# Kernel tuning notes

Hardware: AMD Instinct MI355X
Metric: run time of the kernel (lower is better)

The kernel has to match this reference:

```python
import jax, jax.numpy as jnp
import numpy as np

N = 50000        # nodes
E = 200000       # interior edges
EB = 40000       # boundary edges
WID = 32         # hidden width
KER = 6          # edge feature dim
DEPTH = 4


def setup_inputs() -> dict:
    key = jax.random.key(0)
    ks = jax.random.split(key, 24)
    f32 = jnp.float32

    def nrm(k, sh, s):
        return jax.random.normal(k, sh, dtype=f32) * s

    inp = {
        "x": nrm(ks[0], (N, 1), 1.0),
        "edge_index": jax.random.randint(ks[1], (2, E), 0, N),
        "edge_attr": jax.random.uniform(ks[2], (E, KER), dtype=f32),
        "edge_index_boundary": jax.random.randint(ks[3], (2, EB), 0, N),
        "edge_attr_boundary": jax.random.uniform(ks[4], (EB, KER), dtype=f32),
        # fc1: in_width=1 -> width
        "fc1_w": nrm(ks[5], (1, WID), 0.3), "fc1_b": jnp.zeros((WID,), f32),
        # kernel MLP 1: [6 -> 8 -> 32 -> 32*32], ReLU between layers, none at end
        "k1_w1": nrm(ks[6], (KER, WID // 4), 0.3), "k1_b1": jnp.zeros((WID // 4,), f32),
        "k1_w2": nrm(ks[7], (WID // 4, WID), 0.2), "k1_b2": jnp.zeros((WID,), f32),
        "k1_w3": nrm(ks[8], (WID, WID * WID), 0.05), "k1_b3": jnp.zeros((WID * WID,), f32),
        # kernel MLP 2 (boundary)
        "k2_w1": nrm(ks[9], (KER, WID // 4), 0.3), "k2_b1": jnp.zeros((WID // 4,), f32),
        "k2_w2": nrm(ks[10], (WID // 4, WID), 0.2), "k2_b2": jnp.zeros((WID,), f32),
        "k2_w3": nrm(ks[11], (WID, WID * WID), 0.05), "k2_b3": jnp.zeros((WID * WID,), f32),
        # NNConv root weights + biases
        "root1": nrm(ks[12], (WID, WID), 0.15), "bias1": jnp.zeros((WID,), f32),
        "root2": nrm(ks[13], (WID, WID), 0.15), "bias2": jnp.zeros((WID,), f32),
        # fc2: width -> 1
        "fc2_w": nrm(ks[14], (WID, 1), 0.2), "fc2_b": jnp.zeros((1,), f32),
    }
    return inp


def _kernel_mlp(ea, w1, b1, w2, b2, w3, b3):
    # DenseNet: ReLU between layers, no final nonlinearity -> per-edge [W, W] matrices
    h = jax.nn.relu(ea @ w1 + b1)
    h = jax.nn.relu(h @ w2 + b2)
    return (h @ w3 + b3).reshape(-1, WID, WID)


def _nnconv(x, src, dst, We, root, bias):
    # message: gather x_j then per-edge matmul  [E, W] x [E, W, W] -> [E, W]
    msg = jnp.einsum('ei,eio->eo', x[src], We)
    agg = jax.ops.segment_sum(msg, dst, num_segments=N)
    cnt = jax.ops.segment_sum(jnp.ones((src.shape[0], 1), msg.dtype), dst, num_segments=N)
    mean = agg / jnp.maximum(cnt, 1.0)  # isolated nodes -> 0
    return mean + x @ root + bias


def reference(x, edge_index, edge_attr, edge_index_boundary, edge_attr_boundary,
              fc1_w, fc1_b,
              k1_w1, k1_b1, k1_w2, k1_b2, k1_w3, k1_b3,
              k2_w1, k2_b1, k2_w2, k2_b2, k2_w3, k2_b3,
              root1, bias1, root2, bias2,
              fc2_w, fc2_b):
    src, dst = edge_index[0], edge_index[1]
    srcb, dstb = edge_index_boundary[0], edge_index_boundary[1]
    # edge-conditioned weight matrices are x-independent: hoist out of depth loop
    W1 = _kernel_mlp(edge_attr, k1_w1, k1_b1, k1_w2, k1_b2, k1_w3, k1_b3)
    W2 = _kernel_mlp(edge_attr_boundary, k2_w1, k2_b1, k2_w2, k2_b2, k2_w3, k2_b3)

    h = x @ fc1_w + fc1_b  # [N, W]
    for _ in range(DEPTH):
        h = jax.nn.relu(_nnconv(h, src, dst, W1, root1, bias1)
                        + _nnconv(h, srcb, dstb, W2, root2, bias2))
    return h @ fc2_w + fc2_b  # [N, 1]
```

## Files before the change

### kernel.cpp

```cpp
#include <hip/hip_runtime.h>
#include <hip/hip_bf16.h>

#define WID 32
#define KER 6
#define DEPTH 4
#define WEXT_ELEMS (33 * 2 * 64 * 8)

typedef __attribute__((ext_vector_type(8))) short bf16x8;
typedef __attribute__((ext_vector_type(4))) float f32x4;

static __device__ __forceinline__ float bf2f(unsigned short u) {
  union { unsigned int u; float f; } v; v.u = ((unsigned int)u) << 16; return v.f;
}
static __device__ __forceinline__ unsigned short f2bf(float f) {
  union { float f; unsigned int u; } v; v.f = f;
  unsigned int r = v.u + 0x7fffu + ((v.u >> 16) & 1u);
  return (unsigned short)(r >> 16);
}

__global__ void k_h0(const float* __restrict__ x, const float* __restrict__ w,
                     const float* __restrict__ b, float* __restrict__ h,
                     unsigned short* __restrict__ hbf, int n_nodes) {
  int gid = blockIdx.x * blockDim.x + threadIdx.x;
  if (gid >= n_nodes * WID) return;
  int n = gid >> 5, o = gid & 31;
  float v = x[n] * w[o] + b[o];
  h[gid] = v;
  hbf[gid] = f2bf(v);
}

__global__ void k_cnt(const int* __restrict__ ei, int E,
                      const int* __restrict__ eib, int EB,
                      unsigned int* __restrict__ cnt1, unsigned int* __restrict__ cnt2,
                      unsigned int* __restrict__ rank1, unsigned int* __restrict__ rank2) {
  int idx = blockIdx.x * blockDim.x + threadIdx.x;
  if (idx < E) {
    rank1[idx] = atomicAdd(&cnt1[ei[E + idx]], 1u);
  } else if (idx < E + EB) {
    int e = idx - E;
    rank2[e] = atomicAdd(&cnt2[eib[EB + e]], 1u);
  }
}

__global__ void k_scan1(const unsigned int* __restrict__ cnt, unsigned int* __restrict__ partials,
                        int n2) {
  __shared__ unsigned int s[256];
  int t = threadIdx.x;
  int i = blockIdx.x * 256 + t;
  unsigned int v = (i < n2) ? cnt[i] : 0u;
  s[t] = v;
  __syncthreads();
  for (int d = 128; d > 0; d >>= 1) {
    if (t < d) s[t] += s[t + d];
    __syncthreads();
  }
  if (t == 0) partials[blockIdx.x] = s[0];
}

__global__ void k_scan2(unsigned int* __restrict__ partials, int nb) {
  __shared__ unsigned int s[1024];
  int t = threadIdx.x;
  unsigned int v = (t < nb) ? partials[t] : 0u;
  s[t] = v;
  __syncthreads();
  for (int d = 1; d < 1024; d <<= 1) {
    unsigned int u = (t >= d) ? s[t - d] : 0u;
    __syncthreads();
    s[t] += u;
    __syncthreads();
  }
  if (t < nb) partials[t] = s[t] - v;
}

__global__ void k_scan3(const unsigned int* __restrict__ cnt, const unsigned int* __restrict__ partials,
                        unsigned int* __restrict__ start1, unsigned int* __restrict__ start2,
                        int n, int Etot) {
  __shared__ unsigned int s[256];
  int t = threadIdx.x;
  int i = blockIdx.x * 256 + t;
  int n2 = 2 * n;
  unsigned int v = (i < n2) ? cnt[i] : 0u;
  s[t] = v;
  __syncthreads();
  for (int d = 1; d < 256; d <<= 1) {
    unsigned int u = (t >= d) ? s[t - d] : 0u;
    __syncthreads();
    s[t] += u;
    __syncthreads();
  }
  unsigned int ex = s[t] - v + partials[blockIdx.x];
  if (i < n) start1[i] = ex;
  else if (i < n2) start2[i - n] = ex - (unsigned int)Etot;
}

__global__ void k_edgemlp(const float* __restrict__ ea,
                          const int* __restrict__ eidx, int ecnt,
                          const unsigned int* __restrict__ rank,
                          const unsigned int* __restrict__ start,
                          const float* __restrict__ w1, const float* __restrict__ b1,
                          const float* __restrict__ w2, const float* __restrict__ b2,
                          unsigned short* __restrict__ h3s, int* __restrict__ ssrc) {
  __shared__ float sw1[KER * 8], sb1[8], sw2[8 * WID], sb2[WID];
  int tid = threadIdx.x;
  if (tid < KER * 8) sw1[tid] = w1[tid];
  if (tid < 8) sb1[tid] = b1[tid];
  if (tid < 8 * WID) sw2[tid] = w2[tid];
  if (tid < WID) sb2[tid] = b2[tid];
  __syncthreads();
  int e = blockIdx.x * blockDim.x + tid;
  if (e >= ecnt) return;
  float a[KER];
  #pragma unroll
  for (int i = 0; i < KER; i++) a[i] = ea[e * KER + i];
  float h8[8];
  #pragma unroll
  for (int o = 0; o < 8; o++) {
    float s = sb1[o];
    #pragma unroll
    for (int i = 0; i < KER; i++) s += a[i] * sw1[i * 8 + o];
    h8[o] = fmaxf(s, 0.f);
  }
  int d = eidx[ecnt + e];
  unsigned int p = start[d] + rank[e];
  ssrc[p] = eidx[e];
  size_t base = (size_t)p * WID;
  #pragma unroll
  for (int o = 0; o < WID; o++) {
    float s = sb2[o];
    #pragma unroll
    for (int i = 0; i < 8; i++) s += h8[i] * sw2[i * WID + o];
    h3s[base + o] = f2bf(fmaxf(s, 0.f));
  }
}

__global__ void k_pack2(const float* __restrict__ w3a, const float* __restrict__ b3a,
                        unsigned short* __restrict__ oa,
                        const float* __restrict__ w3b, const float* __restrict__ b3b,
                        unsigned short* __restrict__ ob) {
  int idx = blockIdx.x * blockDim.x + threadIdx.x;
  if (idx >= 2 * WEXT_ELEMS) return;
  int which = idx >= WEXT_ELEMS;
  int id2 = which ? idx - WEXT_ELEMS : idx;
  const float* w3 = which ? w3b : w3a;
  const float* b3 = which ? b3b : b3a;
  unsigned short* outp = which ? ob : oa;
  int j = id2 & 7, l = (id2 >> 3) & 63, tt = (id2 >> 9) & 1, s = id2 >> 10;
  int p = ((l >> 4) << 3) + j;
  int o = tt * 16 + (l & 15);
  float v = (s < 32) ? w3[s * 1024 + p * 32 + o] : b3[p * 32 + o];
  outp[id2] = f2bf(v);
}

__launch_bounds__(512)
__global__ void k_msg2(const unsigned short* __restrict__ hbf,
                       const unsigned short* __restrict__ h3s1, const int* __restrict__ ssrc1,
                       int ecnt1, const unsigned short* __restrict__ w1,
                       unsigned short* __restrict__ msg1,
                       const unsigned short* __restrict__ h3s2, const int* __restrict__ ssrc2,
                       int ecnt2, const unsigned short* __restrict__ w2,
                       unsigned short* __restrict__ msg2, int B1) {
  const unsigned short* h3s; const int* ssrc; const unsigned short* wext;
  unsigned short* msgbuf; int ecnt, blk0, nblk;
  if ((int)blockIdx.x < B1) {
    h3s = h3s1; ssrc = ssrc1; wext = w1; msgbuf = msg1; ecnt = ecnt1;
    blk0 = blockIdx.x; nblk = B1;
  } else {
    h3s = h3s2; ssrc = ssrc2; wext = w2; msgbuf = msg2; ecnt = ecnt2;
    blk0 = blockIdx.x - B1; nblk = gridDim.x - B1;
  }
  __shared__ __align__(16) unsigned short wlds[WEXT_ELEMS];
  {
    const uint4* s4 = (const uint4*)wext;
    uint4* d4 = (uint4*)wlds;
    for (int i = threadIdx.x; i < WEXT_ELEMS / 8; i += blockDim.x) d4[i] = s4[i];
  }
  __syncthreads();
  const int lane = threadIdx.x & 63;
  const int wv = threadIdx.x >> 6;
  const int g = lane >> 4, eo = lane & 15;
  const int ntile = (ecnt + 15) >> 4;
  const int wpb = blockDim.x >> 6;
  const int nwv = nblk * wpb;
  for (int tile = blk0 * wpb + wv; tile < ntile; tile += nwv) {
    const int e = min((tile << 4) + eo, ecnt - 1);
    const int srcn = ssrc[e];
    const uint4* h3p = (const uint4*)(h3s + (size_t)e * WID);
    uint4 q0 = h3p[0], q1 = h3p[1], q2 = h3p[2], q3 = h3p[3];
    unsigned int h3w[16];
    h3w[0]=q0.x; h3w[1]=q0.y; h3w[2]=q0.z; h3w[3]=q0.w;
    h3w[4]=q1.x; h3w[5]=q1.y; h3w[6]=q1.z; h3w[7]=q1.w;
    h3w[8]=q2.x; h3w[9]=q2.y; h3w[10]=q2.z; h3w[11]=q2.w;
    h3w[12]=q3.x; h3w[13]=q3.y; h3w[14]=q3.z; h3w[15]=q3.w;
    uint4 hq = *(const uint4*)(hbf + (size_t)srcn * WID + g * 8);
    bf16x8 hsv = __builtin_bit_cast(bf16x8, hq);
    float hsf[8];
    #pragma unroll
    for (int j = 0; j < 8; j++) hsf[j] = bf2f((unsigned short)hsv[j]);
    f32x4 acc0 = {0.f, 0.f, 0.f, 0.f};
    f32x4 acc1 = {0.f, 0.f, 0.f, 0.f};
    #pragma unroll
    for (int s = 0; s < 32; s++) {
      unsigned int wrd = h3w[s >> 1];
      unsigned int fb = (s & 1) ? (wrd & 0xffff0000u) : (wrd << 16);
      float h3f = __builtin_bit_cast(float, fb);
      float p0 = h3f * hsf[0], p1 = h3f * hsf[1], p2 = h3f * hsf[2], p3 = h3f * hsf[3];
      float p4 = h3f * hsf[4], p5 = h3f * hsf[5], p6 = h3f * hsf[6], p7 = h3f * hsf[7];
      uint4 aw;
      asm("v_cvt_pk_bf16_f32 %0, %1, %2" : "=v"(aw.x) : "v"(p0), "v"(p1));
      asm("v_cvt_pk_bf16_f32 %0, %1, %2" : "=v"(aw.y) : "v"(p2), "v"(p3));
      asm("v_cvt_pk_bf16_f32 %0, %1, %2" : "=v"(aw.z) : "v"(p4), "v"(p5));
      asm("v_cvt_pk_bf16_f32 %0, %1, %2" : "=v"(aw.w) : "v"(p6), "v"(p7));
      bf16x8 af = __builtin_bit_cast(bf16x8, aw);
      bf16x8 b0 = *(const bf16x8*)&wlds[((s * 2 + 0) * 64 + lane) * 8];
      bf16x8 b1 = *(const bf16x8*)&wlds[((s * 2 + 1) * 64 + lane) * 8];
      acc0 = __builtin_amdgcn_mfma_f32_16x16x32_bf16(af, b0, acc0, 0, 0, 0);
      acc1 = __builtin_amdgcn_mfma_f32_16x16x32_bf16(af, b1, acc1, 0, 0, 0);
    }
    {
      bf16x8 b0 = *(const bf16x8*)&wlds[((32 * 2 + 0) * 64 + lane) * 8];
      bf16x8 b1 = *(const bf16x8*)&wlds[((32 * 2 + 1) * 64 + lane) * 8];
      acc0 = __builtin_amdgcn_mfma_f32_16x16x32_bf16(hsv, b0, acc0, 0, 0, 0);
      acc1 = __builtin_amdgcn_mfma_f32_16x16x32_bf16(hsv, b1, acc1, 0, 0, 0);
    }
    #pragma unroll
    for (int r = 0; r < 4; r++) {
      int oe = (tile << 4) + g * 4 + r;
      if (oe < ecnt) {
        msgbuf[(size_t)oe * WID + eo]      = f2bf(acc0[r]);
        msgbuf[(size_t)oe * WID + 16 + eo] = f2bf(acc1[r]);
      }
    }
  }
}

__global__ void k_update(const unsigned short* __restrict__ msg1,
                         const unsigned short* __restrict__ msg2,
                         const unsigned int* __restrict__ start1, const unsigned int* __restrict__ cnt1,
                         const unsigned int* __restrict__ start2, const unsigned int* __restrict__ cnt2,
                         const float* __restrict__ root1, const float* __restrict__ root2,
                         const float* __restrict__ bias1, const float* __restrict__ bias2,
                         float* __restrict__ h, unsigned short* __restrict__ hbf,
                         int last, const float* __restrict__ fc2w, const float* __restrict__ fc2b,
                         float* __restrict__ out, int n_nodes) {
  __shared__ float rs[WID * WID];
  __shared__ float bs[WID];
  __shared__ float hrow[8][WID];
  int tid = threadIdx.x;
  for (int i = tid; i < WID * WID; i += blockDim.x) rs[i] = root1[i] + root2[i];
  if (tid < WID) bs[tid] = bias1[tid] + bias2[tid];
  int o = tid & 31, nl = tid >> 5;
  int n = blockIdx.x * 8 + nl;
  bool ok = (n < n_nodes);
  hrow[nl][o] = ok ? h[(size_t)n * WID + o] : 0.f;
  __syncthreads();
  if (!ok) return;
  unsigned int b1 = start1[n], c1 = cnt1[n];
  unsigned int b2 = start2[n], c2 = cnt2[n];
  float s1 = 0.f, s2 = 0.f;
  for (unsigned int k = 0; k < c1; k++) s1 += bf2f(msg1[(size_t)(b1 + k) * WID + o]);
  for (unsigned int k = 0; k < c2; k++) s2 += bf2f(msg2[(size_t)(b2 + k) * WID + o]);
  float v = s1 / (float)(c1 ? c1 : 1u) + s2 / (float)(c2 ? c2 : 1u) + bs[o];
  #pragma unroll
  for (int i = 0; i < WID; i++) v += hrow[nl][i] * rs[i * WID + o];
  v = fmaxf(v, 0.f);
  h[(size_t)n * WID + o] = v;
  hbf[(size_t)n * WID + o] = f2bf(v);
  if (last) {
    float pv = v * fc2w[o];
    #pragma unroll
    for (int m = 16; m >= 1; m >>= 1) pv += __shfl_xor(pv, m, 32);
    if (o == 0) out[n] = pv + fc2b[0];
  }
}

extern "C" void kernel_launch(void* const* d_in, const int* in_sizes, int n_in,
                              void* d_out, int out_size, void* d_ws, size_t ws_size,
                              hipStream_t stream) {
  const float* x    = (const float*)d_in[0];
  const int*   ei   = (const int*)d_in[1];
  const float* ea   = (const float*)d_in[2];
  const int*   eib  = (const int*)d_in[3];
  const float* eab  = (const float*)d_in[4];
  const float* fc1w = (const float*)d_in[5];
  const float* fc1b = (const float*)d_in[6];
  const float* k1w1 = (const float*)d_in[7];
  const float* k1b1 = (const float*)d_in[8];
  const float* k1w2 = (const float*)d_in[9];
  const float* k1b2 = (const float*)d_in[10];
  const float* k1w3 = (const float*)d_in[11];
  const float* k1b3 = (const float*)d_in[12];
  const float* k2w1 = (const float*)d_in[13];
  const float* k2b1 = (const float*)d_in[14];
  const float* k2w2 = (const float*)d_in[15];
  const float* k2b2 = (const float*)d_in[16];
  const float* k2w3 = (const float*)d_in[17];
  const float* k2b3 = (const float*)d_in[18];
  const float* root1 = (const float*)d_in[19];
  const float* bias1 = (const float*)d_in[20];
  const float* root2 = (const float*)d_in[21];
  const float* bias2 = (const float*)d_in[22];
  const float* fc2w = (const float*)d_in[23];
  const float* fc2b = (const float*)d_in[24];
  float* out = (float*)d_out;

  const int n_nodes = in_sizes[0];
  const int E  = in_sizes[1] / 2;
  const int EB = in_sizes[3] / 2;

  char* ws = (char*)d_ws;
  size_t off = 0;
  auto alloc = [&](size_t bytes) -> void* {
    void* p = ws + off;
    off = (off + bytes + 255) & ~(size_t)255;
    return p;
  };
  unsigned short* h3s1 = (unsigned short*)alloc((size_t)E * WID * 2);
  unsigned short* h3s2 = (unsigned short*)alloc((size_t)EB * WID * 2);
  unsigned short* w1b  = (unsigned short*)alloc((size_t)WEXT_ELEMS * 2);
  unsigned short* w2b  = (unsigned short*)alloc((size_t)WEXT_ELEMS * 2);
  float* h             = (float*)alloc((size_t)n_nodes * WID * 4);
  unsigned short* hbf  = (unsigned short*)alloc((size_t)n_nodes * WID * 2);
  unsigned short* msg1 = (unsigned short*)alloc((size_t)E * WID * 2);
  unsigned short* msg2 = (unsigned short*)alloc((size_t)EB * WID * 2);
  unsigned int* cnt12  = (unsigned int*)alloc((size_t)2 * n_nodes * 4);
  unsigned int* cnt1 = cnt12;
  unsigned int* cnt2 = cnt12 + n_nodes;
  unsigned int* start1 = (unsigned int*)alloc((size_t)n_nodes * 4);
  unsigned int* start2 = (unsigned int*)alloc((size_t)n_nodes * 4);
  unsigned int* rank1  = (unsigned int*)alloc((size_t)E * 4);
  unsigned int* rank2  = (unsigned int*)alloc((size_t)EB * 4);
  int* ssrc1 = (int*)alloc((size_t)E * 4);
  int* ssrc2 = (int*)alloc((size_t)EB * 4);
  unsigned int* partials = (unsigned int*)alloc((size_t)1024 * 4);
  (void)ws_size; (void)n_in; (void)out_size;

  const int n2 = 2 * n_nodes;
  const int nb = (n2 + 255) / 256;

  hipMemsetAsync(cnt12, 0, (size_t)n2 * 4, stream);
  int tot = E + EB;
  k_cnt<<<(tot + 255) / 256, 256, 0, stream>>>(ei, E, eib, EB, cnt1, cnt2, rank1, rank2);
  k_scan1<<<nb, 256, 0, stream>>>(cnt12, partials, n2);
  k_scan2<<<1, 1024, 0, stream>>>(partials, nb);
  k_scan3<<<nb, 256, 0, stream>>>(cnt12, partials, start1, start2, n_nodes, E);
  k_h0<<<(n_nodes * WID + 255) / 256, 256, 0, stream>>>(x, fc1w, fc1b, h, hbf, n_nodes);
  k_edgemlp<<<(E + 255) / 256, 256, 0, stream>>>(ea, ei, E, rank1, start1,
                                                 k1w1, k1b1, k1w2, k1b2, h3s1, ssrc1);
  k_edgemlp<<<(EB + 255) / 256, 256, 0, stream>>>(eab, eib, EB, rank2, start2,
                                                  k2w1, k2b1, k2w2, k2b2, h3s2, ssrc2);
  k_pack2<<<(2 * WEXT_ELEMS + 255) / 256, 256, 0, stream>>>(k1w3, k1b3, w1b, k2w3, k2b3, w2b);

  const int GRID = 512;
  int B1 = (int)(((long long)GRID * E) / (E + EB));
  if (B1 < 1) B1 = 1;
  if (B1 > GRID - 1) B1 = GRID - 1;

  for (int t = 0; t < DEPTH; t++) {
    k_msg2<<<GRID, 512, 0, stream>>>(hbf, h3s1, ssrc1, E, w1b, msg1,
                                     h3s2, ssrc2, EB, w2b, msg2, B1);
    int last = (t == DEPTH - 1);
    k_update<<<(n_nodes + 7) / 8, 256, 0, stream>>>(msg1, msg2, start1, cnt1, start2, cnt2,
                                                    root1, root2, bias1, bias2, h, hbf,
                                                    last, fc2w, fc2b, out, n_nodes);
  }
}
```

Measured before the change: 339.8 us.

## Fuse whole GNN pipeline into cooperative persistent megakernel with grid syncs

Replaces the chain of setup, edge-MLP, pack, message and update kernels with a single cooperative kernel (256 blocks × 512 threads). The phases are separated by grid-wide syncs, and the old launch path is kept as a fallback if the cooperative launch fails. The message stage now processes 32-edge supertiles per wave, sharing the LDS weight fragments across two 16-edge MFMA tiles. The aim is to remove launch gaps and inter-kernel drain between the many small stages. In exchange it adds grid-barrier cost and limits the grid to 256 blocks. The fused update phase also reads h rows from global memory rather than staging them in LDS, which may make it slower than the separate update kernel.

Measured after the change: 854.1 us. 2.51x slower.

```diff
diff --git a/kernel.cpp b/kernel.cpp
--- a/kernel.cpp
+++ b/kernel.cpp
@@ -1,10 +1,15 @@
 #include <hip/hip_runtime.h>
 #include <hip/hip_bf16.h>
+#include <hip/hip_cooperative_groups.h>
+
+namespace cg = cooperative_groups;
 
 #define WID 32
 #define KER 6
 #define DEPTH 4
 #define WEXT_ELEMS (33 * 2 * 64 * 8)
+#define NB 256
+#define NT 512
 
 typedef __attribute__((ext_vector_type(8))) short bf16x8;
 typedef __attribute__((ext_vector_type(4))) float f32x4;
@@ -16,6 +21,271 @@
   union { float f; unsigned int u; } v; v.f = f;
   unsigned int r = v.u + 0x7fffu + ((v.u >> 16) & 1u);
   return (unsigned short)(r >> 16);
+}
+
+static __device__ __forceinline__ void msg_supertile(
+    const unsigned short* __restrict__ hbf, const unsigned short* __restrict__ h3s,
+    const int* __restrict__ ssrc, int ecnt, unsigned short* __restrict__ msgbuf,
+    const unsigned short* wlds, int st, int lane) {
+  const int g = lane >> 4, eo = lane & 15;
+  const int ebase = st * 32;
+  int eA = min(ebase + eo, ecnt - 1);
+  int eB = min(ebase + 16 + eo, ecnt - 1);
+  const uint4* hA = (const uint4*)(h3s + (size_t)eA * WID);
+  const uint4* hB = (const uint4*)(h3s + (size_t)eB * WID);
+  uint4 qa0 = hA[0], qa1 = hA[1], qa2 = hA[2], qa3 = hA[3];
+  uint4 qb0 = hB[0], qb1 = hB[1], qb2 = hB[2], qb3 = hB[3];
+  unsigned int hwA[16], hwB[16];
+  hwA[0]=qa0.x; hwA[1]=qa0.y; hwA[2]=qa0.z; hwA[3]=qa0.w;
+  hwA[4]=qa1.x; hwA[5]=qa1.y; hwA[6]=qa1.z; hwA[7]=qa1.w;
+  hwA[8]=qa2.x; hwA[9]=qa2.y; hwA[10]=qa2.z; hwA[11]=qa2.w;
+  hwA[12]=qa3.x; hwA[13]=qa3.y; hwA[14]=qa3.z; hwA[15]=qa3.w;
+  hwB[0]=qb0.x; hwB[1]=qb0.y; hwB[2]=qb0.z; hwB[3]=qb0.w;
+  hwB[4]=qb1.x; hwB[5]=qb1.y; hwB[6]=qb1.z; hwB[7]=qb1.w;
+  hwB[8]=qb2.x; hwB[9]=qb2.y; hwB[10]=qb2.z; hwB[11]=qb2.w;
+  hwB[12]=qb3.x; hwB[13]=qb3.y; hwB[14]=qb3.z; hwB[15]=qb3.w;
+  int srcA = ssrc[eA], srcB = ssrc[eB];
+  uint4 ha4 = *(const uint4*)(hbf + (size_t)srcA * WID + g * 8);
+  uint4 hb4 = *(const uint4*)(hbf + (size_t)srcB * WID + g * 8);
+  bf16x8 hsvA = __builtin_bit_cast(bf16x8, ha4);
+  bf16x8 hsvB = __builtin_bit_cast(bf16x8, hb4);
+  float hfA[8], hfB[8];
+  #pragma unroll
+  for (int j = 0; j < 8; j++) { hfA[j] = bf2f((unsigned short)hsvA[j]); hfB[j] = bf2f((unsigned short)hsvB[j]); }
+  f32x4 accA0 = {0.f,0.f,0.f,0.f}, accA1 = {0.f,0.f,0.f,0.f};
+  f32x4 accB0 = {0.f,0.f,0.f,0.f}, accB1 = {0.f,0.f,0.f,0.f};
+  #pragma unroll
+  for (int s = 0; s < 32; s++) {
+    unsigned int wa = hwA[s >> 1], wb = hwB[s >> 1];
+    unsigned int fa = (s & 1) ? (wa & 0xffff0000u) : (wa << 16);
+    unsigned int fbm = (s & 1) ? (wb & 0xffff0000u) : (wb << 16);
+    float h3A = __builtin_bit_cast(float, fa);
+    float h3B = __builtin_bit_cast(float, fbm);
+    float a0 = h3A*hfA[0], a1 = h3A*hfA[1], a2 = h3A*hfA[2], a3 = h3A*hfA[3];
+    float a4 = h3A*hfA[4], a5 = h3A*hfA[5], a6 = h3A*hfA[6], a7 = h3A*hfA[7];
+    float c0 = h3B*hfB[0], c1 = h3B*hfB[1], c2 = h3B*hfB[2], c3 = h3B*hfB[3];
+    float c4 = h3B*hfB[4], c5 = h3B*hfB[5], c6 = h3B*hfB[6], c7 = h3B*hfB[7];
+    uint4 awA, awB;
+    asm("v_cvt_pk_bf16_f32 %0, %1, %2" : "=v"(awA.x) : "v"(a0), "v"(a1));
+    asm("v_cvt_pk_bf16_f32 %0, %1, %2" : "=v"(awA.y) : "v"(a2), "v"(a3));
+    asm("v_cvt_pk_bf16_f32 %0, %1, %2" : "=v"(awA.z) : "v"(a4), "v"(a5));
+    asm("v_cvt_pk_bf16_f32 %0, %1, %2" : "=v"(awA.w) : "v"(a6), "v"(a7));
+    asm("v_cvt_pk_bf16_f32 %0, %1, %2" : "=v"(awB.x) : "v"(c0), "v"(c1));
+    asm("v_cvt_pk_bf16_f32 %0, %1, %2" : "=v"(awB.y) : "v"(c2), "v"(c3));
+    asm("v_cvt_pk_bf16_f32 %0, %1, %2" : "=v"(awB.z) : "v"(c4), "v"(c5));
+    asm("v_cvt_pk_bf16_f32 %0, %1, %2" : "=v"(awB.w) : "v"(c6), "v"(c7));
+    bf16x8 afA = __builtin_bit_cast(bf16x8, awA);
+    bf16x8 afB = __builtin_bit_cast(bf16x8, awB);
+    bf16x8 w0 = *(const bf16x8*)&wlds[((s * 2 + 0) * 64 + lane) * 8];
+    bf16x8 w1 = *(const bf16x8*)&wlds[((s * 2 + 1) * 64 + lane) * 8];
+    accA0 = __builtin_amdgcn_mfma_f32_16x16x32_bf16(afA, w0, accA0, 0, 0, 0);
+    accA1 = __builtin_amdgcn_mfma_f32_16x16x32_bf16(afA, w1, accA1, 0, 0, 0);
+    accB0 = __builtin_amdgcn_mfma_f32_16x16x32_bf16(afB, w0, accB0, 0, 0, 0);
+    accB1 = __builtin_amdgcn_mfma_f32_16x16x32_bf16(afB, w1, accB1, 0, 0, 0);
+  }
+  {
+    bf16x8 w0 = *(const bf16x8*)&wlds[((32 * 2 + 0) * 64 + lane) * 8];
+    bf16x8 w1 = *(const bf16x8*)&wlds[((32 * 2 + 1) * 64 + lane) * 8];
+    accA0 = __builtin_amdgcn_mfma_f32_16x16x32_bf16(hsvA, w0, accA0, 0, 0, 0);
+    accA1 = __builtin_amdgcn_mfma_f32_16x16x32_bf16(hsvA, w1, accA1, 0, 0, 0);
+    accB0 = __builtin_amdgcn_mfma_f32_16x16x32_bf16(hsvB, w0, accB0, 0, 0, 0);
+    accB1 = __builtin_amdgcn_mfma_f32_16x16x32_bf16(hsvB, w1, accB1, 0, 0, 0);
+  }
+  #pragma unroll
+  for (int r = 0; r < 4; r++) {
+    int oeA = ebase + g * 4 + r;
+    int oeB = ebase + 16 + g * 4 + r;
+    if (oeA < ecnt) {
+      msgbuf[(size_t)oeA * WID + eo]      = f2bf(accA0[r]);
+      msgbuf[(size_t)oeA * WID + 16 + eo] = f2bf(accA1[r]);
+    }
+    if (oeB < ecnt) {
+      msgbuf[(size_t)oeB * WID + eo]      = f2bf(accB0[r]);
+      msgbuf[(size_t)oeB * WID + 16 + eo] = f2bf(accB1[r]);
+    }
+  }
+}
+
+struct MegaArgs {
+  const float *x; const int *ei; const float *ea; const int *eib; const float *eab;
+  const float *fc1w, *fc1b;
+  const float *k1w1, *k1b1, *k1w2, *k1b2, *k1w3, *k1b3;
+  const float *k2w1, *k2b1, *k2w2, *k2b2, *k2w3, *k2b3;
+  const float *root1, *bias1, *root2, *bias2, *fc2w, *fc2b;
+  float* out;
+  unsigned short *h3s1, *h3s2, *w1b, *w2b, *hbf;
+  float* h;
+  unsigned short *msg1, *msg2;
+  unsigned int *cnt12, *start1, *start2, *rank1, *rank2, *partials;
+  int *ssrc1, *ssrc2;
+  int n_nodes, E, EB, B1;
+};
+
+__launch_bounds__(NT)
+__global__ void k_mega(MegaArgs a) {
+  __shared__ __align__(16) unsigned short wlds[WEXT_ELEMS];
+  __shared__ float rs[WID * WID];
+  __shared__ float bs[WID];
+  __shared__ unsigned int sscan[NT];
+  cg::grid_group grid = cg::this_grid();
+  const int tid = threadIdx.x, bid = blockIdx.x;
+  const int gtid = bid * NT + tid, gsz = NB * NT;
+  const int n_nodes = a.n_nodes, E = a.E, EB = a.EB, B1 = a.B1;
+  const int n2 = 2 * n_nodes;
+
+  for (int i = gtid; i < n2; i += gsz) a.cnt12[i] = 0u;
+  for (int i = gtid; i < n_nodes * WID; i += gsz) {
+    int n = i >> 5, o = i & 31;
+    float v = a.x[n] * a.fc1w[o] + a.fc1b[o];
+    a.h[i] = v; a.hbf[i] = f2bf(v);
+  }
+  for (int i = gtid; i < 2 * WEXT_ELEMS; i += gsz) {
+    int which = i >= WEXT_ELEMS;
+    int id2 = which ? i - WEXT_ELEMS : i;
+    const float* w3 = which ? a.k2w3 : a.k1w3;
+    const float* b3 = which ? a.k2b3 : a.k1b3;
+    unsigned short* outp = which ? a.w2b : a.w1b;
+    int j = id2 & 7, l = (id2 >> 3) & 63, tt = (id2 >> 9) & 1, s = id2 >> 10;
+    int p = ((l >> 4) << 3) + j;
+    int o = tt * 16 + (l & 15);
+    float v = (s < 32) ? w3[s * 1024 + p * 32 + o] : b3[p * 32 + o];
+    outp[id2] = f2bf(v);
+  }
+  for (int i = tid; i < WID * WID; i += NT) rs[i] = a.root1[i] + a.root2[i];
+  if (tid < WID) bs[tid] = a.bias1[tid] + a.bias2[tid];
+  grid.sync();
+
+  for (int i = gtid; i < E + EB; i += gsz) {
+    if (i < E) a.rank1[i] = atomicAdd(&a.cnt12[a.ei[E + i]], 1u);
+    else { int e = i - E; a.rank2[e] = atomicAdd(&a.cnt12[n_nodes + a.eib[EB + e]], 1u); }
+  }
+  grid.sync();
+
+  const int nbS = (n2 + NT - 1) / NT;
+  if (bid < nbS) {
+    int i = bid * NT + tid;
+    unsigned int v = (i < n2) ? a.cnt12[i] : 0u;
+    sscan[tid] = v; __syncthreads();
+    for (int d = NT / 2; d > 0; d >>= 1) { if (tid < d) sscan[tid] += sscan[tid + d]; __syncthreads(); }
+    if (tid == 0) a.partials[bid] = sscan[0];
+  }
+  grid.sync();
+  if (bid == 0) {
+    unsigned int v = (tid < nbS) ? a.partials[tid] : 0u;
+    sscan[tid] = v; __syncthreads();
+    for (int d = 1; d < NT; d <<= 1) { unsigned int u = (tid >= d) ? sscan[tid - d] : 0u; __syncthreads(); sscan[tid] += u; __syncthreads(); }
+    if (tid < nbS) a.partials[tid] = sscan[tid] - v;
+  }
+  grid.sync();
+  if (bid < nbS) {
+    int i = bid * NT + tid;
+    unsigned int v = (i < n2) ? a.cnt12[i] : 0u;
+    sscan[tid] = v; __syncthreads();
+    for (int d = 1; d < NT; d <<= 1) { unsigned int u = (tid >= d) ? sscan[tid - d] : 0u; __syncthreads(); sscan[tid] += u; __syncthreads(); }
+    unsigned int ex = sscan[tid] - v + a.partials[bid];
+    if (i < n_nodes) a.start1[i] = ex;
+    else if (i < n2) a.start2[i - n_nodes] = ex - (unsigned int)E;
+  }
+  grid.sync();
+
+  {
+    bool role1 = bid < B1;
+    const float* w1 = role1 ? a.k1w1 : a.k2w1;
+    const float* b1 = role1 ? a.k1b1 : a.k2b1;
+    const float* w2 = role1 ? a.k1w2 : a.k2w2;
+    const float* b2 = role1 ? a.k1b2 : a.k2b2;
+    float* sw = (float*)sscan;
+    if (tid < KER * 8) sw[tid] = w1[tid];
+    if (tid >= 64 && tid < 72) sw[tid] = b1[tid - 64];
+    if (tid >= 128 && tid < 384) sw[tid] = w2[tid - 128];
+    if (tid >= 384 && tid < 416) sw[tid] = b2[tid - 384];
+    __syncthreads();
+    const int ecnt = role1 ? E : EB;
+    const float* ea = role1 ? a.ea : a.eab;
+    const int* eidx = role1 ? a.ei : a.eib;
+    const unsigned int* rank = role1 ? a.rank1 : a.rank2;
+    const unsigned int* start = role1 ? a.start1 : a.start2;
+    unsigned short* h3s = role1 ? a.h3s1 : a.h3s2;
+    int* ssrc = role1 ? a.ssrc1 : a.ssrc2;
+    int blk0 = role1 ? bid : bid - B1;
+    int rblocks = role1 ? B1 : NB - B1;
+    for (int e = blk0 * NT + tid; e < ecnt; e += rblocks * NT) {
+      float aa[KER];
+      #pragma unroll
+      for (int i = 0; i < KER; i++) aa[i] = ea[e * KER + i];
+      float h8[8];
+      #pragma unroll
+      for (int o = 0; o < 8; o++) {
+        float s = sw[64 + o];
+        #pragma unroll
+        for (int i = 0; i < KER; i++) s += aa[i] * sw[i * 8 + o];
+        h8[o] = fmaxf(s, 0.f);
+      }
+      int d = eidx[ecnt + e];
+      unsigned int p = start[d] + rank[e];
+      ssrc[p] = eidx[e];
+      size_t base = (size_t)p * WID;
+      #pragma unroll
+      for (int o = 0; o < WID; o++) {
+        float s = sw[384 + o];
+        #pragma unroll
+        for (int i = 0; i < 8; i++) s += h8[i] * sw[128 + i * 32 + o];
+        h3s[base + o] = f2bf(fmaxf(s, 0.f));
+      }
+    }
+  }
+  grid.sync();
+
+  {
+    const unsigned short* wsrc = (bid < B1) ? a.w1b : a.w2b;
+    const uint4* s4 = (const uint4*)wsrc;
+    uint4* d4 = (uint4*)wlds;
+    for (int i = tid; i < WEXT_ELEMS / 8; i += NT) d4[i] = s4[i];
+  }
+  __syncthreads();
+
+  const int lane = tid & 63, wv = tid >> 6;
+  for (int t = 0; t < DEPTH; t++) {
+    {
+      bool role1 = bid < B1;
+      const unsigned short* h3s = role1 ? a.h3s1 : a.h3s2;
+      const int* ssrc = role1 ? a.ssrc1 : a.ssrc2;
+      unsigned short* msgbuf = role1 ? a.msg1 : a.msg2;
+      int ecnt = role1 ? E : EB;
+      int blk0 = role1 ? bid : bid - B1;
+      int rblocks = role1 ? B1 : NB - B1;
+      int nst = (ecnt + 31) >> 5;
+      int wpb = NT >> 6, nwv = rblocks * wpb;
+      for (int st = blk0 * wpb + wv; st < nst; st += nwv)
+        msg_supertile(a.hbf, h3s, ssrc, ecnt, msgbuf, wlds, st, lane);
+    }
+    grid.sync();
+    {
+      int last = (t == DEPTH - 1);
+      for (int idx = gtid; idx < n_nodes * WID; idx += gsz) {
+        int n = idx >> 5, o = idx & 31;
+        unsigned int b1v = a.start1[n], c1v = a.cnt12[n];
+        unsigned int b2v = a.start2[n], c2v = a.cnt12[n_nodes + n];
+        float s1 = 0.f, s2 = 0.f;
+        for (unsigned int k = 0; k < c1v; k++) s1 += bf2f(a.msg1[(size_t)(b1v + k) * WID + o]);
+        for (unsigned int k = 0; k < c2v; k++) s2 += bf2f(a.msg2[(size_t)(b2v + k) * WID + o]);
+        float v = s1 / (float)(c1v ? c1v : 1u) + s2 / (float)(c2v ? c2v : 1u) + bs[o];
+        const float* hrow = a.h + (size_t)n * WID;
+        #pragma unroll
+        for (int i = 0; i < WID; i++) v += hrow[i] * rs[i * WID + o];
+        v = fmaxf(v, 0.f);
+        a.h[idx] = v;
+        a.hbf[idx] = f2bf(v);
+        if (last) {
+          float pv = v * a.fc2w[o];
+          #pragma unroll
+          for (int m = 16; m >= 1; m >>= 1) pv += __shfl_xor(pv, m, 32);
+          if (o == 0) a.out[n] = pv + a.fc2b[0];
+        }
+      }
+    }
+    if (t < DEPTH - 1) grid.sync();
+  }
 }
 
 __global__ void k_h0(const float* __restrict__ x, const float* __restrict__ w,
@@ -158,15 +428,15 @@
                        unsigned short* __restrict__ msg1,
                        const unsigned short* __restrict__ h3s2, const int* __restrict__ ssrc2,
                        int ecnt2, const unsigned short* __restrict__ w2,
-                       unsigned short* __restrict__ msg2, int B1) {
+                       unsigned short* __restrict__ msg2, int B1f) {
   const unsigned short* h3s; const int* ssrc; const unsigned short* wext;
   unsigned short* msgbuf; int ecnt, blk0, nblk;
-  if ((int)blockIdx.x < B1) {
+  if ((int)blockIdx.x < B1f) {
     h3s = h3s1; ssrc = ssrc1; wext = w1; msgbuf = msg1; ecnt = ecnt1;
-    blk0 = blockIdx.x; nblk = B1;
+    blk0 = blockIdx.x; nblk = B1f;
   } else {
     h3s = h3s2; ssrc = ssrc2; wext = w2; msgbuf = msg2; ecnt = ecnt2;
-    blk0 = blockIdx.x - B1; nblk = gridDim.x - B1;
+    blk0 = blockIdx.x - B1f; nblk = gridDim.x - B1f;
   }
   __shared__ __align__(16) unsigned short wlds[WEXT_ELEMS];
   {
@@ -177,60 +447,11 @@
   __syncthreads();
   const int lane = threadIdx.x & 63;
   const int wv = threadIdx.x >> 6;
-  const int g = lane >> 4, eo = lane & 15;
-  const int ntile = (ecnt + 15) >> 4;
+  const int nst = (ecnt + 31) >> 5;
   const int wpb = blockDim.x >> 6;
   const int nwv = nblk * wpb;
-  for (int tile = blk0 * wpb + wv; tile < ntile; tile += nwv) {
-    const int e = min((tile << 4) + eo, ecnt - 1);
-    const int srcn = ssrc[e];
-    const uint4* h3p = (const uint4*)(h3s + (size_t)e * WID);
-    uint4 q0 = h3p[0], q1 = h3p[1], q2 = h3p[2], q3 = h3p[3];
-    unsigned int h3w[16];
-    h3w[0]=q0.x; h3w[1]=q0.y; h3w[2]=q0.z; h3w[3]=q0.w;
-    h3w[4]=q1.x; h3w[5]=q1.y; h3w[6]=q1.z; h3w[7]=q1.w;
-    h3w[8]=q2.x; h3w[9]=q2.y; h3w[10]=q2.z; h3w[11]=q2.w;
-    h3w[12]=q3.x; h3w[13]=q3.y; h3w[14]=q3.z; h3w[15]=q3.w;
-    uint4 hq = *(const uint4*)(hbf + (size_t)srcn * WID + g * 8);
-    bf16x8 hsv = __builtin_bit_cast(bf16x8, hq);
-    float hsf[8];
-    #pragma unroll
-    for (int j = 0; j < 8; j++) hsf[j] = bf2f((unsigned short)hsv[j]);
-    f32x4 acc0 = {0.f, 0.f, 0.f, 0.f};
-    f32x4 acc1 = {0.f, 0.f, 0.f, 0.f};
-    #pragma unroll
-    for (int s = 0; s < 32; s++) {
-      unsigned int wrd = h3w[s >> 1];
-      unsigned int fb = (s & 1) ? (wrd & 0xffff0000u) : (wrd << 16);
-      float h3f = __builtin_bit_cast(float, fb);
-      float p0 = h3f * hsf[0], p1 = h3f * hsf[1], p2 = h3f * hsf[2], p3 = h3f * hsf[3];
-      float p4 = h3f * hsf[4], p5 = h3f * hsf[5], p6 = h3f * hsf[6], p7 = h3f * hsf[7];
-      uint4 aw;
-      asm("v_cvt_pk_bf16_f32 %0, %1, %2" : "=v"(aw.x) : "v"(p0), "v"(p1));
-      asm("v_cvt_pk_bf16_f32 %0, %1, %2" : "=v"(aw.y) : "v"(p2), "v"(p3));
-      asm("v_cvt_pk_bf16_f32 %0, %1, %2" : "=v"(aw.z) : "v"(p4), "v"(p5));
-      asm("v_cvt_pk_bf16_f32 %0, %1, %2" : "=v"(aw.w) : "v"(p6), "v"(p7));
-      bf16x8 af = __builtin_bit_cast(bf16x8, aw);
-      bf16x8 b0 = *(const bf16x8*)&wlds[((s * 2 + 0) * 64 + lane) * 8];
-      bf16x8 b1 = *(const bf16x8*)&wlds[((s * 2 + 1) * 64 + lane) * 8];
-      acc0 = __builtin_amdgcn_mfma_f32_16x16x32_bf16(af, b0, acc0, 0, 0, 0);
-      acc1 = __builtin_amdgcn_mfma_f32_16x16x32_bf16(af, b1, acc1, 0, 0, 0);
-    }
-    {
-      bf16x8 b0 = *(const bf16x8*)&wlds[((32 * 2 + 0) * 64 + lane) * 8];
-      bf16x8 b1 = *(const bf16x8*)&wlds[((32 * 2 + 1) * 64 + lane) * 8];
-      acc0 = __builtin_amdgcn_mfma_f32_16x16x32_bf16(hsv, b0, acc0, 0, 0, 0);
-      acc1 = __builtin_amdgcn_mfma_f32_16x16x32_bf16(hsv, b1, acc1, 0, 0, 0);
-    }
-    #pragma unroll
-    for (int r = 0; r < 4; r++) {
-      int oe = (tile << 4) + g * 4 + r;
-      if (oe < ecnt) {
-        msgbuf[(size_t)oe * WID + eo]      = f2bf(acc0[r]);
-        msgbuf[(size_t)oe * WID + 16 + eo] = f2bf(acc1[r]);
-      }
-    }
-  }
+  for (int st = blk0 * wpb + wv; st < nst; st += nwv)
+    msg_supertile(hbf, h3s, ssrc, ecnt, msgbuf, wlds, st, lane);
 }
 
 __global__ void k_update(const unsigned short* __restrict__ msg1,
@@ -334,9 +555,32 @@
   unsigned int* partials = (unsigned int*)alloc((size_t)1024 * 4);
   (void)ws_size; (void)n_in; (void)out_size;
 
+  int B1c = (int)(((long long)NB * E) / (E + EB));
+  if (B1c < 1) B1c = 1;
+  if (B1c > NB - 1) B1c = NB - 1;
+
+  MegaArgs ma;
+  ma.x = x; ma.ei = ei; ma.ea = ea; ma.eib = eib; ma.eab = eab;
+  ma.fc1w = fc1w; ma.fc1b = fc1b;
+  ma.k1w1 = k1w1; ma.k1b1 = k1b1; ma.k1w2 = k1w2; ma.k1b2 = k1b2; ma.k1w3 = k1w3; ma.k1b3 = k1b3;
+  ma.k2w1 = k2w1; ma.k2b1 = k2b1; ma.k2w2 = k2w2; ma.k2b2 = k2b2; ma.k2w3 = k2w3; ma.k2b3 = k2b3;
+  ma.root1 = root1; ma.bias1 = bias1; ma.root2 = root2; ma.bias2 = bias2;
+  ma.fc2w = fc2w; ma.fc2b = fc2b; ma.out = out;
+  ma.h3s1 = h3s1; ma.h3s2 = h3s2; ma.w1b = w1b; ma.w2b = w2b; ma.hbf = hbf;
+  ma.h = h; ma.msg1 = msg1; ma.msg2 = msg2;
+  ma.cnt12 = cnt12; ma.start1 = start1; ma.start2 = start2;
+  ma.rank1 = rank1; ma.rank2 = rank2; ma.partials = partials;
+  ma.ssrc1 = ssrc1; ma.ssrc2 = ssrc2;
+  ma.n_nodes = n_nodes; ma.E = E; ma.EB = EB; ma.B1 = B1c;
+
+  void* kargs[] = { (void*)&ma };
+  hipError_t cerr = hipLaunchCooperativeKernel(reinterpret_cast<const void*>(&k_mega),
+                                               dim3(NB), dim3(NT), kargs, 0, stream);
+  if (cerr == hipSuccess) return;
+  (void)hipGetLastError();
+
   const int n2 = 2 * n_nodes;
   const int nb = (n2 + 255) / 256;
-
   hipMemsetAsync(cnt12, 0, (size_t)n2 * 4, stream);
   int tot = E + EB;
   k_cnt<<<(tot + 255) / 256, 256, 0, stream>>>(ei, E, eib, EB, cnt1, cnt2, rank1, rank2);
@@ -351,13 +595,13 @@
   k_pack2<<<(2 * WEXT_ELEMS + 255) / 256, 256, 0, stream>>>(k1w3, k1b3, w1b, k2w3, k2b3, w2b);
 
   const int GRID = 512;
-  int B1 = (int)(((long long)GRID * E) / (E + EB));
-  if (B1 < 1) B1 = 1;
-  if (B1 > GRID - 1) B1 = GRID - 1;
+  int B1f = (int)(((long long)GRID * E) / (E + EB));
+  if (B1f < 1) B1f = 1;
+  if (B1f > GRID - 1) B1f = GRID - 1;
 
   for (int t = 0; t < DEPTH; t++) {
     k_msg2<<<GRID, 512, 0, stream>>>(hbf, h3s1, ssrc1, E, w1b, msg1,
-                                     h3s2, ssrc2, EB, w2b, msg2, B1);
+                                     h3s2, ssrc2, EB, w2b, msg2, B1f);
     int last = (t == DEPTH - 1);
     k_update<<<(n_nodes + 7) / 8, 256, 0, stream>>>(msg1, msg2, start1, cnt1, start2, cnt2,
                                                     root1, root2, bias1, bias2, h, hbf,
```
